# Optimization experiments

Measured on AMD Instinct MI355X. Metric: run time of the kernel, lower is better.

The kernel has to match this reference:

```python
import jax, jax.numpy as jnp
import numpy as np

N = 100000      # nodes
F_IN = 256      # num_node_features
E = 1600000     # edges (before self-loops)
DIMS = [F_IN, 128, 100, 32, 2]  # GCNConv layer widths


def _glorot(key, fan_in, fan_out):
    s = jnp.sqrt(6.0 / (fan_in + fan_out))
    return jax.random.uniform(key, (fan_in, fan_out), jnp.float32, -s, s)


def setup_inputs() -> dict:
    key = jax.random.key(0)
    ks = jax.random.split(key, 10)
    x = jax.random.normal(ks[0], (N, F_IN), jnp.float32)
    edge_index = jax.random.randint(ks[1], (2, E), 0, N, jnp.int32)
    inp = {"x": x, "edge_index": edge_index}
    for i in range(4):
        inp[f"W{i+1}"] = _glorot(ks[2 + 2 * i], DIMS[i], DIMS[i + 1])
        inp[f"b{i+1}"] = jnp.zeros((DIMS[i + 1],), jnp.float32)
    return inp


def reference(x, edge_index, W1, b1, W2, b2, W3, b3, W4, b4):
    n = x.shape[0]
    loops = jnp.arange(n, dtype=edge_index.dtype)
    src = jnp.concatenate([edge_index[0], loops])  # [E+N]
    dst = jnp.concatenate([edge_index[1], loops])
    # symmetric normalization: deg^-1/2[src] * deg^-1/2[dst] (self-loops included)
    deg = jax.ops.segment_sum(jnp.ones_like(src, x.dtype), dst, num_segments=n)
    dis = jax.lax.rsqrt(jnp.maximum(deg, 1.0))
    norm = (dis[src] * dis[dst])[:, None]  # [E+N, 1]

    def conv(h, W, b):
        h = h @ W                                      # [N, out]
        msg = h[src] * norm                            # gather + scale [E+N, out]
        return jax.ops.segment_sum(msg, dst, num_segments=n) + b

    h = jax.nn.leaky_relu(conv(x, W1, b1), negative_slope=0.1)
    h = jax.nn.leaky_relu(conv(h, W2, b2), negative_slope=0.1)
    h = jax.nn.leaky_relu(conv(h, W3, b3), negative_slope=0.1)
    h = conv(h, W4, b4)
    return jax.nn.softmax(h, axis=-1)
```

## Files before the change

### kernel.cpp

```cpp
#include <hip/hip_runtime.h>
#include <math.h>


typedef unsigned short ushort_t;
typedef unsigned int   uint_t;
typedef short  bf16x8 __attribute__((ext_vector_type(8)));
typedef float  f32x4  __attribute__((ext_vector_type(4)));

#define BKT_SHIFT 8
#define BKT_CAP   5120
#define BIN_CHUNK 4096

__device__ __forceinline__ ushort_t f2bf(float f) {
    union { float f; uint_t u; } v; v.f = f;
    uint_t u = v.u;
    u += 0x7fffu + ((u >> 16) & 1u);
    return (ushort_t)(u >> 16);
}
__device__ __forceinline__ float bflo(uint_t u) {
    union { uint_t q; float f; } v; v.q = u << 16; return v.f;
}
__device__ __forceinline__ float bfhi(uint_t u) {
    union { uint_t q; float f; } v; v.q = u & 0xffff0000u; return v.f;
}


__global__ __launch_bounds__(256) void bin_kernel(const int* __restrict__ srcArr,
                                                  const int* __restrict__ dstArr,
                                                  int* __restrict__ bkt_cursor,
                                                  uint2* __restrict__ staging,
                                                  int E, int nb) {
    __shared__ int hist[512];
    __shared__ int base[512];
    for (int b = threadIdx.x; b < 512; b += 256) hist[b] = 0;
    __syncthreads();
    const int e0 = blockIdx.x * BIN_CHUNK;
    #pragma unroll 4
    for (int k = 0; k < BIN_CHUNK / 256; ++k) {
        int e = e0 + k * 256 + threadIdx.x;
        if (e < E) atomicAdd(&hist[dstArr[e] >> BKT_SHIFT], 1);
    }
    __syncthreads();
    for (int b = threadIdx.x; b < nb; b += 256) {
        int h = hist[b];
        base[b] = h ? atomicAdd(&bkt_cursor[b], h) : 0;
    }
    __syncthreads();
    for (int b = threadIdx.x; b < 512; b += 256) hist[b] = 0;
    __syncthreads();
    #pragma unroll 4
    for (int k = 0; k < BIN_CHUNK / 256; ++k) {
        int e = e0 + k * 256 + threadIdx.x;
        if (e < E) {
            int s = srcArr[e], d = dstArr[e];
            int b = d >> BKT_SHIFT;
            int p = atomicAdd(&hist[b], 1);
            int idx = base[b] + p;
            if (idx < BKT_CAP)
                staging[(size_t)b * BKT_CAP + idx] = make_uint2((uint_t)s, (uint_t)d);
        }
    }
}

__global__ __launch_bounds__(256) void deg_from_staging_kernel(const uint2* __restrict__ staging,
                                                               const int* __restrict__ bkt_cursor,
                                                               int* __restrict__ degi,
                                                               float* __restrict__ dis, int n) {
    __shared__ int cur[256];
    const int b  = blockIdx.x;
    const int lo = b << BKT_SHIFT;
    const int nl = min(256, n - lo);
    cur[threadIdx.x] = 0;
    __syncthreads();
    int cnt = min(bkt_cursor[b], BKT_CAP);
    for (int e = threadIdx.x; e < cnt; e += 256) {
        uint2 p = staging[(size_t)b * BKT_CAP + e];
        atomicAdd(&cur[(int)p.y - lo], 1);
    }
    __syncthreads();
    if ((int)threadIdx.x < nl) {
        int d = cur[threadIdx.x];
        degi[lo + threadIdx.x] = d;
        dis[lo + threadIdx.x] = rsqrtf((float)(d + 1));
    }
}

__global__ void scan_block_kernel(const int* __restrict__ degi, int* __restrict__ row_excl,
                                  int* __restrict__ bsums, int n) {
    __shared__ int buf[1024];
    int i = blockIdx.x * 1024 + threadIdx.x;
    int v = (i < n) ? degi[i] : 0;
    buf[threadIdx.x] = v;
    __syncthreads();
    for (int off = 1; off < 1024; off <<= 1) {
        int t = (threadIdx.x >= (unsigned)off) ? buf[threadIdx.x - off] : 0;
        __syncthreads();
        buf[threadIdx.x] += t;
        __syncthreads();
    }
    if (i < n) row_excl[i] = buf[threadIdx.x] - v;
    if (threadIdx.x == 1023) bsums[blockIdx.x] = buf[1023];
}

__global__ void scan_sums_kernel(int* __restrict__ bsums, int nb) {
    __shared__ int buf[128];
    int v = ((int)threadIdx.x < nb) ? bsums[threadIdx.x] : 0;
    buf[threadIdx.x] = v;
    __syncthreads();
    for (int off = 1; off < 128; off <<= 1) {
        int t = (threadIdx.x >= (unsigned)off) ? buf[threadIdx.x - off] : 0;
        __syncthreads();
        buf[threadIdx.x] += t;
        __syncthreads();
    }
    if ((int)threadIdx.x < nb) bsums[threadIdx.x] = buf[threadIdx.x] - v;
    if (threadIdx.x == 0) bsums[nb] = buf[127];
}

__global__ void scan_add_kernel(int* __restrict__ row_start, const int* __restrict__ bsums,
                                int n, int nb) {
    int i = blockIdx.x * blockDim.x + threadIdx.x;
    if (i < n) row_start[i] += bsums[i >> 10];
    else if (i == n) row_start[n] = bsums[nb];
}

__global__ __launch_bounds__(256) void csr_build_kernel(const uint2* __restrict__ staging,
                                                        const int* __restrict__ bkt_cursor,
                                                        const int* __restrict__ row_start,
                                                        int* __restrict__ csr_src, int n) {
    __shared__ int rs[257];
    __shared__ int cur[256];
    __shared__ int seg[BKT_CAP];
    const int b  = blockIdx.x;
    const int lo = b << BKT_SHIFT;
    const int nl = min(256, n - lo);
    if ((int)threadIdx.x <= nl) rs[threadIdx.x] = row_start[lo + threadIdx.x];
    cur[threadIdx.x] = 0;
    __syncthreads();
    const int sbase = rs[0];
    int cnt = min(bkt_cursor[b], BKT_CAP);
    for (int e = threadIdx.x; e < cnt; e += 256) {
        uint2 p = staging[(size_t)b * BKT_CAP + e];
        int ln = (int)p.y - lo;
        int q  = atomicAdd(&cur[ln], 1);
        seg[(rs[ln] - sbase) + q] = (int)p.x;
    }
    __syncthreads();
    for (int i = threadIdx.x; i < cnt; i += 256) csr_src[sbase + i] = seg[i];
}


__global__ void cast_bf16_kernel(const float* __restrict__ in, ushort_t* __restrict__ out, int n8) {
    int i = blockIdx.x * blockDim.x + threadIdx.x;
    if (i >= n8) return;
    const float4 f0 = ((const float4*)in)[2 * i];
    const float4 f1 = ((const float4*)in)[2 * i + 1];
    uint4 o;
    o.x = (uint_t)f2bf(f0.x) | ((uint_t)f2bf(f0.y) << 16);
    o.y = (uint_t)f2bf(f0.z) | ((uint_t)f2bf(f0.w) << 16);
    o.z = (uint_t)f2bf(f1.x) | ((uint_t)f2bf(f1.y) << 16);
    o.w = (uint_t)f2bf(f1.z) | ((uint_t)f2bf(f1.w) << 16);
    ((uint4*)out)[i] = o;
}

__global__ void wt_all_kernel(const float* __restrict__ W1, const float* __restrict__ W2,
                              const float* __restrict__ W3,
                              ushort_t* __restrict__ Wt1, ushort_t* __restrict__ Wt2,
                              ushort_t* __restrict__ Wt3) {
    int idx = blockIdx.x * blockDim.x + threadIdx.x;
    if (idx < 32768) {
        int nn = idx >> 8, k = idx & 255;
        Wt1[idx] = f2bf(W1[(size_t)k * 128 + nn]);
    } else if (idx < 49152) {
        int j = idx - 32768;
        int nn = j >> 7, k = j & 127;
        float v = (nn < 100) ? W2[(size_t)k * 100 + nn] : 0.f;
        Wt2[j] = f2bf(v);
    } else if (idx < 57344) {
        int j = idx - 49152;
        int nn = j >> 7, k = j & 127;
        float v = (k < 100 && nn < 32) ? W3[(size_t)k * 32 + nn] : 0.f;
        Wt3[j] = f2bf(v);
    }
}

template <int NFR>
__global__ __launch_bounds__(256) void gemm_tile(const ushort_t* __restrict__ A,
                                                 const ushort_t* __restrict__ Bt,
                                                 ushort_t* __restrict__ C,
                                                 const float* __restrict__ dis,
                                                 int M, int K, int lda, int ldb, int ldc) {
    constexpr int BN = NFR * 32;
    __shared__ __attribute__((aligned(16))) ushort_t As[64][72];
    __shared__ __attribute__((aligned(16))) ushort_t Bs[BN][72];

    const int t    = threadIdx.x;
    const int lane = t & 63;
    const int w    = t >> 6;
    const int wm   = w >> 1, wn = w & 1;
    const int m0   = blockIdx.x * 64;
    const int rsel = lane & 15;
    const int q    = lane >> 4;

    f32x4 acc[2][NFR];
    #pragma unroll
    for (int mi = 0; mi < 2; ++mi)
        #pragma unroll
        for (int ni = 0; ni < NFR; ++ni) acc[mi][ni] = (f32x4){0.f, 0.f, 0.f, 0.f};

    const int srow = t >> 3;
    const int scol = (t & 7) * 8;

    for (int k0 = 0; k0 < K; k0 += 64) {
        #pragma unroll
        for (int it = 0; it < 2; ++it) {
            int r = srow + it * 32;
            int gm = m0 + r;
            bf16x8 v = {0, 0, 0, 0, 0, 0, 0, 0};
            if (gm < M) v = *(const bf16x8*)(A + (size_t)gm * lda + k0 + scol);
            *(bf16x8*)&As[r][scol] = v;
        }
        #pragma unroll
        for (int it = 0; it < BN / 32; ++it) {
            int r = srow + it * 32;
            bf16x8 v = *(const bf16x8*)(Bt + (size_t)r * ldb + k0 + scol);
            *(bf16x8*)&Bs[r][scol] = v;
        }
        __syncthreads();
        #pragma unroll
        for (int ks = 0; ks < 2; ++ks) {
            const int kc = ks * 32 + q * 8;
            bf16x8 af[2], bfr[NFR];
            #pragma unroll
            for (int mi = 0; mi < 2; ++mi)
                af[mi] = *(const bf16x8*)&As[wm * 32 + mi * 16 + rsel][kc];
            #pragma unroll
            for (int ni = 0; ni < NFR; ++ni)
                bfr[ni] = *(const bf16x8*)&Bs[wn * (BN / 2) + ni * 16 + rsel][kc];
            #pragma unroll
            for (int mi = 0; mi < 2; ++mi)
                #pragma unroll
                for (int ni = 0; ni < NFR; ++ni)
                    acc[mi][ni] = __builtin_amdgcn_mfma_f32_16x16x32_bf16(
                        bfr[ni], af[mi], acc[mi][ni], 0, 0, 0);
        }
        __syncthreads();
    }

    #pragma unroll
    for (int mi = 0; mi < 2; ++mi) {
        const int gm = m0 + wm * 32 + mi * 16 + rsel;
        if (gm >= M) continue;
        const float d = dis[gm];
        #pragma unroll
        for (int ni = 0; ni < NFR; ++ni) {
            uint2 o;
            o.x = (uint_t)f2bf(acc[mi][ni][0] * d) | ((uint_t)f2bf(acc[mi][ni][1] * d) << 16);
            o.y = (uint_t)f2bf(acc[mi][ni][2] * d) | ((uint_t)f2bf(acc[mi][ni][3] * d) << 16);
            *(uint2*)(C + (size_t)gm * ldc + wn * (BN / 2) + ni * 16 + q * 4) = o;
        }
    }
}

template <int F>
__global__ void aggregate128_kernel(const ushort_t* __restrict__ h, const int* __restrict__ row_start,
                                    const int* __restrict__ csr_src,
                                    const float* __restrict__ dis, const float* __restrict__ bias,
                                    ushort_t* __restrict__ out, int n) {
    int wid  = threadIdx.x >> 6;
    int lane = threadIdx.x & 63;
    int node = blockIdx.x * 4 + wid;
    if (node >= n) return;
    const int q  = lane >> 4;
    const int fb = (lane & 15) * 8;
    float a[8];
    #pragma unroll
    for (int j = 0; j < 8; ++j) a[j] = 0.f;

    int i = row_start[node], end = row_start[node + 1];

#define ACC8(U)                                                     \
    do {                                                            \
        a[0] += bflo((U).x); a[1] += bfhi((U).x);                   \
        a[2] += bflo((U).y); a[3] += bfhi((U).y);                   \
        a[4] += bflo((U).z); a[5] += bfhi((U).z);                   \
        a[6] += bflo((U).w); a[7] += bfhi((U).w);                   \
    } while (0)

    #pragma unroll 2
    for (; i + 8 <= end; i += 8) {
        int sA = csr_src[i + q];
        int sB = csr_src[i + 4 + q];
        uint4 u = *(const uint4*)(h + (size_t)sA * 128 + fb);
        uint4 v = *(const uint4*)(h + (size_t)sB * 128 + fb);
        ACC8(u);
        ACC8(v);
    }
    int r = end - i;
    if (r > 0) {
        if (q < r) {
            int sA = csr_src[i + q];
            uint4 u = *(const uint4*)(h + (size_t)sA * 128 + fb);
            ACC8(u);
        }
        if (q + 4 < r) {
            int sB = csr_src[i + 4 + q];
            uint4 v = *(const uint4*)(h + (size_t)sB * 128 + fb);
            ACC8(v);
        }
    }
#undef ACC8

    #pragma unroll
    for (int j = 0; j < 8; ++j) {
        a[j] += __shfl_xor(a[j], 16);
        a[j] += __shfl_xor(a[j], 32);
    }

    if (q == 0) {
        uint4 su = *(const uint4*)(h + (size_t)node * 128 + fb);
        a[0] += bflo(su.x); a[1] += bfhi(su.x);
        a[2] += bflo(su.y); a[3] += bfhi(su.y);
        a[4] += bflo(su.z); a[5] += bfhi(su.z);
        a[6] += bflo(su.w); a[7] += bfhi(su.w);
        float dn = dis[node];
        #pragma unroll
        for (int j = 0; j < 8; ++j) {
            float b = (fb + j < F) ? bias[fb + j] : 0.f;
            float v = a[j] * dn + b;
            v = (v > 0.f) ? v : 0.1f * v;
            if (fb + j >= F) v = 0.f;
            a[j] = v;
        }
        uint4 o;
        o.x = (uint_t)f2bf(a[0]) | ((uint_t)f2bf(a[1]) << 16);
        o.y = (uint_t)f2bf(a[2]) | ((uint_t)f2bf(a[3]) << 16);
        o.z = (uint_t)f2bf(a[4]) | ((uint_t)f2bf(a[5]) << 16);
        o.w = (uint_t)f2bf(a[6]) | ((uint_t)f2bf(a[7]) << 16);
        *(uint4*)(out + (size_t)node * 128 + fb) = o;
    }
}

__global__ void aggregate32_kernel(const ushort_t* __restrict__ h, const int* __restrict__ row_start,
                                   const int* __restrict__ csr_src,
                                   const float* __restrict__ dis, const float* __restrict__ bias,
                                   ushort_t* __restrict__ out, int n) {
    int lane16 = threadIdx.x & 15;
    int node = blockIdx.x * (blockDim.x >> 4) + (threadIdx.x >> 4);
    if (node >= n) return;
    const int f0 = 2 * lane16;
    uint_t v = *(const uint_t*)(h + (size_t)node * 32 + f0);
    float acc0 = bflo(v);
    float acc1 = bfhi(v);
    int i = row_start[node], end = row_start[node + 1];
    for (; i + 4 <= end; i += 4) {
        int s0 = csr_src[i], s1 = csr_src[i + 1], s2 = csr_src[i + 2], s3 = csr_src[i + 3];
        uint_t u0 = *(const uint_t*)(h + (size_t)s0 * 32 + f0);
        uint_t u1 = *(const uint_t*)(h + (size_t)s1 * 32 + f0);
        uint_t u2 = *(const uint_t*)(h + (size_t)s2 * 32 + f0);
        uint_t u3 = *(const uint_t*)(h + (size_t)s3 * 32 + f0);
        acc0 += bflo(u0) + bflo(u1) + bflo(u2) + bflo(u3);
        acc1 += bfhi(u0) + bfhi(u1) + bfhi(u2) + bfhi(u3);
    }
    for (; i < end; ++i) {
        int s = csr_src[i];
        uint_t u = *(const uint_t*)(h + (size_t)s * 32 + f0);
        acc0 += bflo(u); acc1 += bfhi(u);
    }
    float dn = dis[node];
    acc0 = acc0 * dn + bias[f0];
    acc1 = acc1 * dn + bias[f0 + 1];
    acc0 = (acc0 > 0.f) ? acc0 : 0.1f * acc0;
    acc1 = (acc1 > 0.f) ? acc1 : 0.1f * acc1;
    uint_t o = (uint_t)f2bf(acc0) | ((uint_t)f2bf(acc1) << 16);
    *(uint_t*)(out + (size_t)node * 32 + f0) = o;
}

__global__ void gemm32x2_kernel(const ushort_t* __restrict__ H, const float* __restrict__ W4,
                                const float* __restrict__ dis, float* __restrict__ C, int n) {
    int node = blockIdx.x * blockDim.x + threadIdx.x;
    if (node >= n) return;
    const uint_t* row = (const uint_t*)(H + (size_t)node * 32);
    float a0 = 0.f, a1 = 0.f;
    #pragma unroll
    for (int k2 = 0; k2 < 16; ++k2) {
        uint_t u = row[k2];
        float x0 = bflo(u), x1 = bfhi(u);
        int k = 2 * k2;
        a0 += x0 * W4[k * 2]     + x1 * W4[(k + 1) * 2];
        a1 += x0 * W4[k * 2 + 1] + x1 * W4[(k + 1) * 2 + 1];
    }
    float d = dis[node];
    C[2 * (size_t)node]     = a0 * d;
    C[2 * (size_t)node + 1] = a1 * d;
}

__global__ void aggregate2_softmax_kernel(const float* __restrict__ h, const int* __restrict__ row_start,
                                          const int* __restrict__ csr_src,
                                          const float* __restrict__ dis, const float* __restrict__ bias,
                                          float* __restrict__ out, int n) {
    int node = blockIdx.x * blockDim.x + threadIdx.x;
    if (node >= n) return;
    float a0 = h[2 * (size_t)node];
    float a1 = h[2 * (size_t)node + 1];
    int beg = row_start[node], end = row_start[node + 1];
    for (int i = beg; i < end; ++i) {
        int s = csr_src[i];
        a0 += h[2 * (size_t)s];
        a1 += h[2 * (size_t)s + 1];
    }
    float dn = dis[node];
    a0 = a0 * dn + bias[0];
    a1 = a1 * dn + bias[1];
    float m  = fmaxf(a0, a1);
    float e0 = expf(a0 - m), e1 = expf(a1 - m);
    float inv = 1.f / (e0 + e1);
    out[2 * (size_t)node]     = e0 * inv;
    out[2 * (size_t)node + 1] = e1 * inv;
}


extern "C" void kernel_launch(void* const* d_in, const int* in_sizes, int n_in,
                              void* d_out, int out_size, void* d_ws, size_t ws_size,
                              hipStream_t stream) {
    const float* x  = (const float*)d_in[0];
    const int*   ei = (const int*)d_in[1];
    const float* W1 = (const float*)d_in[2];
    const float* b1 = (const float*)d_in[3];
    const float* W2 = (const float*)d_in[4];
    const float* b2 = (const float*)d_in[5];
    const float* W3 = (const float*)d_in[6];
    const float* b3 = (const float*)d_in[7];
    const float* W4 = (const float*)d_in[8];
    const float* b4 = (const float*)d_in[9];

    const int N = in_sizes[0] / 256;
    const int E = in_sizes[1] / 2;
    const int* srcA = ei;
    const int* dstA = ei + E;
    const int nbkt = (N + 255) >> BKT_SHIFT;

    char* ws = (char*)d_ws;
    size_t off = 0;
    auto alloc = [&](size_t bytes) {
        void* p = ws + off;
        off = (off + bytes + 255) & ~(size_t)255;
        return p;
    };
    int*      degi       = (int*)alloc((size_t)N * 4);
    float*    dis        = (float*)alloc((size_t)N * 4);
    int*      row_start  = (int*)alloc((size_t)(N + 1) * 4);
    int*      bsums      = (int*)alloc(512 * 4);
    int*      bkt_cursor = (int*)alloc((size_t)nbkt * 4);
    int*      csr_src    = (int*)alloc((size_t)E * 4);
    uint2*    staging    = (uint2*)alloc((size_t)nbkt * BKT_CAP * 8);
    ushort_t* xb         = (ushort_t*)alloc((size_t)N * 256 * 2);
    ushort_t* bufA       = (ushort_t*)alloc((size_t)N * 128 * 2);
    ushort_t* bufB       = (ushort_t*)alloc((size_t)N * 128 * 2);
    float*    C4         = (float*)alloc((size_t)N * 2 * 4);
    ushort_t* Wt1        = (ushort_t*)alloc((size_t)128 * 256 * 2);
    ushort_t* Wt2        = (ushort_t*)alloc((size_t)128 * 128 * 2);
    ushort_t* Wt3        = (ushort_t*)alloc((size_t)64 * 128 * 2);
    (void)ws_size;

    hipMemsetAsync(bkt_cursor, 0, (size_t)nbkt * 4, stream);

    bin_kernel<<<(E + BIN_CHUNK - 1) / BIN_CHUNK, 256, 0, stream>>>(
        srcA, dstA, bkt_cursor, staging, E, nbkt);
    deg_from_staging_kernel<<<nbkt, 256, 0, stream>>>(staging, bkt_cursor, degi, dis, N);
    const int nb = (N + 1023) >> 10;
    scan_block_kernel<<<nb, 1024, 0, stream>>>(degi, row_start, bsums, N);
    scan_sums_kernel<<<1, 128, 0, stream>>>(bsums, nb);
    scan_add_kernel<<<(N + 256) / 256, 256, 0, stream>>>(row_start, bsums, N, nb);
    csr_build_kernel<<<nbkt, 256, 0, stream>>>(staging, bkt_cursor, row_start, csr_src, N);

    wt_all_kernel<<<(57344 + 255) / 256, 256, 0, stream>>>(W1, W2, W3, Wt1, Wt2, Wt3);
    const int n8 = N * 32;
    cast_bf16_kernel<<<(n8 + 255) / 256, 256, 0, stream>>>(x, xb, n8);

    const int gx = (N + 63) / 64;
    const int aggBlocks128 = (N + 3) / 4;
    const int aggBlocks32  = (N + 15) / 16;

    gemm_tile<4><<<gx, 256, 0, stream>>>(xb, Wt1, bufA, dis, N, 256, 256, 256, 128);
    aggregate128_kernel<128><<<aggBlocks128, 256, 0, stream>>>(
        bufA, row_start, csr_src, dis, b1, bufB, N);
    gemm_tile<4><<<gx, 256, 0, stream>>>(bufB, Wt2, bufA, dis, N, 128, 128, 128, 128);
    aggregate128_kernel<100><<<aggBlocks128, 256, 0, stream>>>(
        bufA, row_start, csr_src, dis, b2, bufB, N);
    gemm_tile<1><<<gx, 256, 0, stream>>>(bufB, Wt3, bufA, dis, N, 128, 128, 128, 32);
    aggregate32_kernel<<<aggBlocks32, 256, 0, stream>>>(
        bufA, row_start, csr_src, dis, b3, bufB, N);
    gemm32x2_kernel<<<(N + 255) / 256, 256, 0, stream>>>(bufB, W4, dis, C4, N);
    aggregate2_softmax_kernel<<<(N + 255) / 256, 256, 0, stream>>>(
        C4, row_start, csr_src, dis, b4, (float*)d_out, N);
}
```

Measured before the change: 317.4 us.

## Fuse degree count, row scan and CSR build into bucket-level scan pipeline

Replaces the separate degree, three-stage global scan and CSR build kernels with a single-block scan over bucket counts followed by one per-bucket kernel. That kernel counts degrees, does a local prefix scan, writes row_start and dis, and scatters sources into the CSR. This removes three kernel launches and one extra pass over the staging buffer. It also switches the aggregation kernels to 32-bit byte-offset addressing to cut 64-bit index arithmetic, which assumes the feature buffers stay under 4 GB.

```diff
diff --git a/kernel.cpp b/kernel.cpp
--- a/kernel.cpp
+++ b/kernel.cpp
@@ -62,91 +62,71 @@
     }
 }
 
-__global__ __launch_bounds__(256) void deg_from_staging_kernel(const uint2* __restrict__ staging,
-                                                               const int* __restrict__ bkt_cursor,
-                                                               int* __restrict__ degi,
-                                                               float* __restrict__ dis, int n) {
-    __shared__ int cur[256];
+__global__ __launch_bounds__(512) void bucket_scan_kernel(const int* __restrict__ bkt_cursor,
+                                                          int* __restrict__ bkt_base,
+                                                          int* __restrict__ row_start,
+                                                          int nbkt, int n) {
+    __shared__ int buf[512];
+    int v = ((int)threadIdx.x < nbkt) ? min(bkt_cursor[threadIdx.x], BKT_CAP) : 0;
+    buf[threadIdx.x] = v;
+    __syncthreads();
+    for (int off = 1; off < 512; off <<= 1) {
+        int t = (threadIdx.x >= (unsigned)off) ? buf[threadIdx.x - off] : 0;
+        __syncthreads();
+        buf[threadIdx.x] += t;
+        __syncthreads();
+    }
+    if ((int)threadIdx.x < nbkt) bkt_base[threadIdx.x] = buf[threadIdx.x] - v;
+    if ((int)threadIdx.x == nbkt - 1) row_start[n] = buf[threadIdx.x];
+}
+
+__global__ __launch_bounds__(256) void csr_build2_kernel(const uint2* __restrict__ staging,
+                                                         const int* __restrict__ bkt_cursor,
+                                                         const int* __restrict__ bkt_base,
+                                                         int* __restrict__ row_start,
+                                                         float* __restrict__ dis,
+                                                         int* __restrict__ csr_src, int n) {
+    __shared__ int cnt[256];
+    __shared__ int buf[256];
+    __shared__ int rsS[256];
+    __shared__ int seg[BKT_CAP];
+    const int t  = threadIdx.x;
     const int b  = blockIdx.x;
     const int lo = b << BKT_SHIFT;
     const int nl = min(256, n - lo);
-    cur[threadIdx.x] = 0;
-    __syncthreads();
-    int cnt = min(bkt_cursor[b], BKT_CAP);
-    for (int e = threadIdx.x; e < cnt; e += 256) {
+    cnt[t] = 0;
+    __syncthreads();
+    const int cntE = min(bkt_cursor[b], BKT_CAP);
+    for (int e = t; e < cntE; e += 256) {
         uint2 p = staging[(size_t)b * BKT_CAP + e];
-        atomicAdd(&cur[(int)p.y - lo], 1);
-    }
-    __syncthreads();
-    if ((int)threadIdx.x < nl) {
-        int d = cur[threadIdx.x];
-        degi[lo + threadIdx.x] = d;
-        dis[lo + threadIdx.x] = rsqrtf((float)(d + 1));
-    }
-}
-
-__global__ void scan_block_kernel(const int* __restrict__ degi, int* __restrict__ row_excl,
-                                  int* __restrict__ bsums, int n) {
-    __shared__ int buf[1024];
-    int i = blockIdx.x * 1024 + threadIdx.x;
-    int v = (i < n) ? degi[i] : 0;
-    buf[threadIdx.x] = v;
-    __syncthreads();
-    for (int off = 1; off < 1024; off <<= 1) {
-        int t = (threadIdx.x >= (unsigned)off) ? buf[threadIdx.x - off] : 0;
-        __syncthreads();
-        buf[threadIdx.x] += t;
-        __syncthreads();
-    }
-    if (i < n) row_excl[i] = buf[threadIdx.x] - v;
-    if (threadIdx.x == 1023) bsums[blockIdx.x] = buf[1023];
-}
-
-__global__ void scan_sums_kernel(int* __restrict__ bsums, int nb) {
-    __shared__ int buf[128];
-    int v = ((int)threadIdx.x < nb) ? bsums[threadIdx.x] : 0;
-    buf[threadIdx.x] = v;
-    __syncthreads();
-    for (int off = 1; off < 128; off <<= 1) {
-        int t = (threadIdx.x >= (unsigned)off) ? buf[threadIdx.x - off] : 0;
-        __syncthreads();
-        buf[threadIdx.x] += t;
-        __syncthreads();
-    }
-    if ((int)threadIdx.x < nb) bsums[threadIdx.x] = buf[threadIdx.x] - v;
-    if (threadIdx.x == 0) bsums[nb] = buf[127];
-}
-
-__global__ void scan_add_kernel(int* __restrict__ row_start, const int* __restrict__ bsums,
-                                int n, int nb) {
-    int i = blockIdx.x * blockDim.x + threadIdx.x;
-    if (i < n) row_start[i] += bsums[i >> 10];
-    else if (i == n) row_start[n] = bsums[nb];
-}
-
-__global__ __launch_bounds__(256) void csr_build_kernel(const uint2* __restrict__ staging,
-                                                        const int* __restrict__ bkt_cursor,
-                                                        const int* __restrict__ row_start,
-                                                        int* __restrict__ csr_src, int n) {
-    __shared__ int rs[257];
-    __shared__ int cur[256];
-    __shared__ int seg[BKT_CAP];
-    const int b  = blockIdx.x;
-    const int lo = b << BKT_SHIFT;
-    const int nl = min(256, n - lo);
-    if ((int)threadIdx.x <= nl) rs[threadIdx.x] = row_start[lo + threadIdx.x];
-    cur[threadIdx.x] = 0;
-    __syncthreads();
-    const int sbase = rs[0];
-    int cnt = min(bkt_cursor[b], BKT_CAP);
-    for (int e = threadIdx.x; e < cnt; e += 256) {
+        atomicAdd(&cnt[(int)p.y - lo], 1);
+    }
+    __syncthreads();
+    const int v = cnt[t];
+    buf[t] = v;
+    __syncthreads();
+    for (int off = 1; off < 256; off <<= 1) {
+        int tt = (t >= off) ? buf[t - off] : 0;
+        __syncthreads();
+        buf[t] += tt;
+        __syncthreads();
+    }
+    rsS[t] = buf[t] - v;
+    const int sbase = bkt_base[b];
+    if (t < nl) {
+        row_start[lo + t] = sbase + (buf[t] - v);
+        dis[lo + t] = rsqrtf((float)(v + 1));
+    }
+    cnt[t] = 0;
+    __syncthreads();
+    for (int e = t; e < cntE; e += 256) {
         uint2 p = staging[(size_t)b * BKT_CAP + e];
         int ln = (int)p.y - lo;
-        int q  = atomicAdd(&cur[ln], 1);
-        seg[(rs[ln] - sbase) + q] = (int)p.x;
-    }
-    __syncthreads();
-    for (int i = threadIdx.x; i < cnt; i += 256) csr_src[sbase + i] = seg[i];
+        int q  = atomicAdd(&cnt[ln], 1);
+        seg[rsS[ln] + q] = (int)p.x;
+    }
+    __syncthreads();
+    for (int i = t; i < cntE; i += 256) csr_src[sbase + i] = seg[i];
 }
 
 
@@ -271,14 +251,16 @@
     int lane = threadIdx.x & 63;
     int node = blockIdx.x * 4 + wid;
     if (node >= n) return;
-    const int q  = lane >> 4;
-    const int fb = (lane & 15) * 8;
+    const int q    = lane >> 4;
+    const uint_t fbb = (uint_t)(lane & 15) << 4;
+    const char* hb = (const char*)h;
     float a[8];
     #pragma unroll
     for (int j = 0; j < 8; ++j) a[j] = 0.f;
 
     int i = row_start[node], end = row_start[node + 1];
 
+#define LOADR(S) (*(const uint4*)(hb + (((uint_t)(S) << 8) + fbb)))
 #define ACC8(U)                                                     \
     do {                                                            \
         a[0] += bflo((U).x); a[1] += bfhi((U).x);                   \
@@ -291,25 +273,22 @@
     for (; i + 8 <= end; i += 8) {
         int sA = csr_src[i + q];
         int sB = csr_src[i + 4 + q];
-        uint4 u = *(const uint4*)(h + (size_t)sA * 128 + fb);
-        uint4 v = *(const uint4*)(h + (size_t)sB * 128 + fb);
+        uint4 u = LOADR(sA);
+        uint4 v = LOADR(sB);
         ACC8(u);
         ACC8(v);
     }
     int r = end - i;
     if (r > 0) {
         if (q < r) {
-            int sA = csr_src[i + q];
-            uint4 u = *(const uint4*)(h + (size_t)sA * 128 + fb);
+            uint4 u = LOADR(csr_src[i + q]);
             ACC8(u);
         }
         if (q + 4 < r) {
-            int sB = csr_src[i + 4 + q];
-            uint4 v = *(const uint4*)(h + (size_t)sB * 128 + fb);
+            uint4 v = LOADR(csr_src[i + 4 + q]);
             ACC8(v);
         }
     }
-#undef ACC8
 
     #pragma unroll
     for (int j = 0; j < 8; ++j) {
@@ -318,12 +297,10 @@
     }
 
     if (q == 0) {
-        uint4 su = *(const uint4*)(h + (size_t)node * 128 + fb);
-        a[0] += bflo(su.x); a[1] += bfhi(su.x);
-        a[2] += bflo(su.y); a[3] += bfhi(su.y);
-        a[4] += bflo(su.z); a[5] += bfhi(su.z);
-        a[6] += bflo(su.w); a[7] += bfhi(su.w);
+        uint4 su = LOADR(node);
+        ACC8(su);
         float dn = dis[node];
+        const int fb = (lane & 15) * 8;
         #pragma unroll
         for (int j = 0; j < 8; ++j) {
             float b = (fb + j < F) ? bias[fb + j] : 0.f;
@@ -337,8 +314,10 @@
         o.y = (uint_t)f2bf(a[2]) | ((uint_t)f2bf(a[3]) << 16);
         o.z = (uint_t)f2bf(a[4]) | ((uint_t)f2bf(a[5]) << 16);
         o.w = (uint_t)f2bf(a[6]) | ((uint_t)f2bf(a[7]) << 16);
-        *(uint4*)(out + (size_t)node * 128 + fb) = o;
-    }
+        *(uint4*)((char*)out + (((uint_t)node << 8) + fbb)) = o;
+    }
+#undef ACC8
+#undef LOADR
 }
 
 __global__ void aggregate32_kernel(const ushort_t* __restrict__ h, const int* __restrict__ row_start,
@@ -348,32 +327,34 @@
     int lane16 = threadIdx.x & 15;
     int node = blockIdx.x * (blockDim.x >> 4) + (threadIdx.x >> 4);
     if (node >= n) return;
-    const int f0 = 2 * lane16;
-    uint_t v = *(const uint_t*)(h + (size_t)node * 32 + f0);
+    const uint_t fbb = (uint_t)lane16 << 2;
+    const char* hb = (const char*)h;
+#define LOADR32(S) (*(const uint_t*)(hb + (((uint_t)(S) << 6) + fbb)))
+    uint_t v = LOADR32(node);
     float acc0 = bflo(v);
     float acc1 = bfhi(v);
     int i = row_start[node], end = row_start[node + 1];
     for (; i + 4 <= end; i += 4) {
-        int s0 = csr_src[i], s1 = csr_src[i + 1], s2 = csr_src[i + 2], s3 = csr_src[i + 3];
-        uint_t u0 = *(const uint_t*)(h + (size_t)s0 * 32 + f0);
-        uint_t u1 = *(const uint_t*)(h + (size_t)s1 * 32 + f0);
-        uint_t u2 = *(const uint_t*)(h + (size_t)s2 * 32 + f0);
-        uint_t u3 = *(const uint_t*)(h + (size_t)s3 * 32 + f0);
+        uint_t u0 = LOADR32(csr_src[i]);
+        uint_t u1 = LOADR32(csr_src[i + 1]);
+        uint_t u2 = LOADR32(csr_src[i + 2]);
+        uint_t u3 = LOADR32(csr_src[i + 3]);
         acc0 += bflo(u0) + bflo(u1) + bflo(u2) + bflo(u3);
         acc1 += bfhi(u0) + bfhi(u1) + bfhi(u2) + bfhi(u3);
     }
     for (; i < end; ++i) {
-        int s = csr_src[i];
-        uint_t u = *(const uint_t*)(h + (size_t)s * 32 + f0);
+        uint_t u = LOADR32(csr_src[i]);
         acc0 += bflo(u); acc1 += bfhi(u);
     }
+#undef LOADR32
     float dn = dis[node];
+    const int f0 = 2 * lane16;
     acc0 = acc0 * dn + bias[f0];
     acc1 = acc1 * dn + bias[f0 + 1];
     acc0 = (acc0 > 0.f) ? acc0 : 0.1f * acc0;
     acc1 = (acc1 > 0.f) ? acc1 : 0.1f * acc1;
     uint_t o = (uint_t)f2bf(acc0) | ((uint_t)f2bf(acc1) << 16);
-    *(uint_t*)(out + (size_t)node * 32 + f0) = o;
+    *(uint_t*)((char*)out + (((uint_t)node << 6) + fbb)) = o;
 }
 
 __global__ void gemm32x2_kernel(const ushort_t* __restrict__ H, const float* __restrict__ W4,
@@ -401,13 +382,15 @@
                                           float* __restrict__ out, int n) {
     int node = blockIdx.x * blockDim.x + threadIdx.x;
     if (node >= n) return;
+    const char* hb = (const char*)h;
     float a0 = h[2 * (size_t)node];
     float a1 = h[2 * (size_t)node + 1];
     int beg = row_start[node], end = row_start[node + 1];
     for (int i = beg; i < end; ++i) {
-        int s = csr_src[i];
-        a0 += h[2 * (size_t)s];
-        a1 += h[2 * (size_t)s + 1];
+        uint_t off = (uint_t)csr_src[i] << 3;
+        float2 u = *(const float2*)(hb + off);
+        a0 += u.x;
+        a1 += u.y;
     }
     float dn = dis[node];
     a0 = a0 * dn + bias[0];
@@ -447,11 +430,10 @@
         off = (off + bytes + 255) & ~(size_t)255;
         return p;
     };
-    int*      degi       = (int*)alloc((size_t)N * 4);
     float*    dis        = (float*)alloc((size_t)N * 4);
     int*      row_start  = (int*)alloc((size_t)(N + 1) * 4);
-    int*      bsums      = (int*)alloc(512 * 4);
-    int*      bkt_cursor = (int*)alloc((size_t)nbkt * 4);
+    int*      bkt_cursor = (int*)alloc(512 * 4);
+    int*      bkt_base   = (int*)alloc(512 * 4);
     int*      csr_src    = (int*)alloc((size_t)E * 4);
     uint2*    staging    = (uint2*)alloc((size_t)nbkt * BKT_CAP * 8);
     ushort_t* xb         = (ushort_t*)alloc((size_t)N * 256 * 2);
@@ -463,16 +445,13 @@
     ushort_t* Wt3        = (ushort_t*)alloc((size_t)64 * 128 * 2);
     (void)ws_size;
 
-    hipMemsetAsync(bkt_cursor, 0, (size_t)nbkt * 4, stream);
+    hipMemsetAsync(bkt_cursor, 0, 512 * 4, stream);
 
     bin_kernel<<<(E + BIN_CHUNK - 1) / BIN_CHUNK, 256, 0, stream>>>(
         srcA, dstA, bkt_cursor, staging, E, nbkt);
-    deg_from_staging_kernel<<<nbkt, 256, 0, stream>>>(staging, bkt_cursor, degi, dis, N);
-    const int nb = (N + 1023) >> 10;
-    scan_block_kernel<<<nb, 1024, 0, stream>>>(degi, row_start, bsums, N);
-    scan_sums_kernel<<<1, 128, 0, stream>>>(bsums, nb);
-    scan_add_kernel<<<(N + 256) / 256, 256, 0, stream>>>(row_start, bsums, N, nb);
-    csr_build_kernel<<<nbkt, 256, 0, stream>>>(staging, bkt_cursor, row_start, csr_src, N);
+    bucket_scan_kernel<<<1, 512, 0, stream>>>(bkt_cursor, bkt_base, row_start, nbkt, N);
+    csr_build2_kernel<<<nbkt, 256, 0, stream>>>(staging, bkt_cursor, bkt_base,
+                                                row_start, dis, csr_src, N);
 
     wt_all_kernel<<<(57344 + 255) / 256, 256, 0, stream>>>(W1, W2, W3, Wt1, Wt2, Wt3);
     const int n8 = N * 32;
```

New measurement: 299.9 us. 5.5% less time.
